# Optimization experiments

Measured on AMD Instinct MI355X. Metric: run time of the kernel, lower is better.

The kernel has to match this reference:

```python
import jax, jax.numpy as jnp
import numpy as np

V, D, B, S, T, MAXLEN = 32000, 256, 4, 512, 256, 512


def _gru(x, Wih, Whh, bih, bhh):
    """torch-style GRU over x:[B,L,Din] -> [B,L,D]. Weight rows ordered [r,z,n]."""
    Dh = Whh.shape[1]
    xW = x @ Wih.T + bih  # [B,L,3D] precompute input projections

    def step(h, xw):
        hW = h @ Whh.T + bhh
        xr, xz, xn = jnp.split(xw, 3, axis=-1)
        hr, hz, hn = jnp.split(hW, 3, axis=-1)
        r = jax.nn.sigmoid(xr + hr)
        z = jax.nn.sigmoid(xz + hz)
        n = jnp.tanh(xn + r * hn)
        h = (1.0 - z) * n + z * h
        return h, h

    h0 = jnp.zeros((x.shape[0], Dh), x.dtype)
    _, ys = jax.lax.scan(step, h0, jnp.swapaxes(xW, 0, 1))
    return jnp.swapaxes(ys, 0, 1)


def setup_inputs() -> dict:
    key = jax.random.key(0)
    ks = jax.random.split(key, 24)

    def n(k, shape, scale=0.02):
        return (jax.random.normal(k, shape, jnp.float32) * scale).astype(jnp.float32)

    inp = {
        "src": jax.random.randint(ks[0], (B, S), 0, V),
        "tgt": jax.random.randint(ks[1], (B, T), 0, V),
        "emb": n(ks[2], (V, D)),
        "pos": n(ks[3], (MAXLEN, D)),
        # encoder forward direction
        "ef_wih": n(ks[4], (3 * D, D)), "ef_whh": n(ks[5], (3 * D, D)),
        "ef_bih": n(ks[6], (3 * D,)), "ef_bhh": n(ks[7], (3 * D,)),
        # encoder backward direction
        "eb_wih": n(ks[8], (3 * D, D)), "eb_whh": n(ks[9], (3 * D, D)),
        "eb_bih": n(ks[10], (3 * D,)), "eb_bhh": n(ks[11], (3 * D,)),
        # decoder
        "d_wih": n(ks[12], (3 * D, D)), "d_whh": n(ks[13], (3 * D, D)),
        "d_bih": n(ks[14], (3 * D,)), "d_bhh": n(ks[15], (3 * D,)),
        "Wq": n(ks[16], (D, D)),
        "Wk": n(ks[17], (D, 2 * D)),
        "Wgen": n(ks[18], (V, 3 * D)), "bgen": n(ks[19], (V,)),
        "Wgate": n(ks[20], (1, 3 * D)), "bgate": n(ks[21], (1,)),
    }
    return inp


def reference(src, tgt, emb, pos,
              ef_wih, ef_whh, ef_bih, ef_bhh,
              eb_wih, eb_whh, eb_bih, eb_bhh,
              d_wih, d_whh, d_bih, d_bhh,
              Wq, Wk, Wgen, bgen, Wgate, bgate):
    b, s = src.shape
    t = tgt.shape[1]
    d = emb.shape[1]
    v = emb.shape[0]

    src_emb = emb[src] + pos[:s][None]          # [B,S,D]
    enc_f = _gru(src_emb, ef_wih, ef_whh, ef_bih, ef_bhh)
    enc_b = _gru(src_emb[:, ::-1], eb_wih, eb_whh, eb_bih, eb_bhh)[:, ::-1]
    enc_out = jnp.concatenate([enc_f, enc_b], axis=-1)  # [B,S,2D]

    tgt_emb = emb[tgt] + pos[:t][None]
    dec_out = _gru(tgt_emb, d_wih, d_whh, d_bih, d_bhh)  # [B,T,D]

    Q = dec_out @ Wq.T                           # [B,T,D]
    K = enc_out @ Wk.T                           # [B,S,D]
    scores = jnp.einsum('btd,bsd->bts', Q, K) / jnp.sqrt(jnp.asarray(d, jnp.float32))
    pos_probs = jax.nn.softmax(scores, axis=-1)  # [B,T,S]

    # copy distribution: scatter attention mass into vocab buckets (== one_hot bmm)
    P_copy = jnp.zeros((b, t, v), pos_probs.dtype).at[
        jnp.arange(b)[:, None, None],
        jnp.arange(t)[None, :, None],
        src[:, None, :],
    ].add(pos_probs)

    ctx_f = jnp.einsum('bts,bsd->btd', pos_probs, enc_f)
    ctx_b = jnp.einsum('bts,bsd->btd', pos_probs, enc_b)
    combined = jnp.concatenate([dec_out, ctx_f, ctx_b], axis=-1)  # [B,T,3D]

    P_gen = jax.nn.softmax(combined @ Wgen.T + bgen, axis=-1)     # [B,T,V]
    gate = jax.nn.sigmoid(combined @ Wgate.T + bgate)             # [B,T,1]
    return gate * P_gen + (1.0 - gate) * P_copy
```

## Files before the change

### kernel.cpp

```cpp
#include <hip/hip_runtime.h>
#include <hip/hip_bf16.h>
#include <math.h>

#define VV   32000
#define DIM  256
#define BB   4
#define SS   512
#define TT   256
#define D2   512
#define D3   768

typedef __attribute__((ext_vector_type(8))) short s16x8;
typedef __attribute__((ext_vector_type(4))) float f32x4;

__device__ __forceinline__ float rcp_(float x) { return __builtin_amdgcn_rcpf(x); }
__device__ __forceinline__ float sigmoidf_(float x) { return rcp_(1.0f + __expf(-x)); }
__device__ __forceinline__ float tanhf_(float x) {
    float t = __expf(-2.0f * x);
    return (1.0f - t) * rcp_(1.0f + t);
}
__device__ __forceinline__ short f2bf(float f) {
    unsigned u = __float_as_uint(f);
    u += 0x7FFFu + ((u >> 16) & 1u);
    return (short)(u >> 16);
}

#define BAR_LGKM() asm volatile("s_waitcnt lgkmcnt(0)\n\ts_barrier" ::: "memory")

__global__ __launch_bounds__(256) void k_embed(const int* __restrict__ src,
                                               const int* __restrict__ tgt,
                                               const float* __restrict__ emb,
                                               const float* __restrict__ pos,
                                               float* __restrict__ src_emb,
                                               float* __restrict__ tgt_emb) {
    int i = blockIdx.x * 256 + threadIdx.x;
    const int nS = BB * SS * DIM;
    if (i < nS) {
        int d = i & (DIM - 1);
        int s = (i >> 8) & (SS - 1);
        int b = i >> 17;
        src_emb[i] = emb[(size_t)src[b * SS + s] * DIM + d] + pos[s * DIM + d];
    } else {
        int j = i - nS;
        int d = j & (DIM - 1);
        int t = (j >> 8) & (TT - 1);
        int b = j >> 16;
        tgt_emb[j] = emb[(size_t)tgt[b * TT + t] * DIM + d] + pos[t * DIM + d];
    }
}

struct GDesc {
    const float* A; int lda;
    const float* Bt; int ldb;
    const float* bias;
    float* C; int ldc;
    int M, N;
};

#define BMM 128
#define BNN 128
#define BKK 8

__global__ __launch_bounds__(256) void k_gemmb(GDesc d0, GDesc d1, GDesc d2) {
    GDesc d = (blockIdx.z == 0) ? d0 : ((blockIdx.z == 1) ? d1 : d2);
    int brow = blockIdx.y * BMM, bcol = blockIdx.x * BNN;
    if (brow >= d.M || bcol >= d.N) return;

    __shared__ float As[BKK][BMM + 4];
    __shared__ float Bs[BKK][BNN + 4];
    const int K = d.lda;
    int tid = threadIdx.x;
    int tx = tid & 15, ty = tid >> 4;
    float acc[8][8];
#pragma unroll
    for (int i = 0; i < 8; i++)
#pragma unroll
        for (int j = 0; j < 8; j++) acc[i][j] = 0.0f;

    int lr = tid >> 1;
    int lk = (tid & 1) * 4;
    for (int k0 = 0; k0 < K; k0 += BKK) {
        float4 a4 = *(const float4*)&d.A[(size_t)(brow + lr) * d.lda + k0 + lk];
        float4 b4 = *(const float4*)&d.Bt[(size_t)(bcol + lr) * d.ldb + k0 + lk];
        As[lk + 0][lr] = a4.x; As[lk + 1][lr] = a4.y; As[lk + 2][lr] = a4.z; As[lk + 3][lr] = a4.w;
        Bs[lk + 0][lr] = b4.x; Bs[lk + 1][lr] = b4.y; Bs[lk + 2][lr] = b4.z; Bs[lk + 3][lr] = b4.w;
        __syncthreads();
#pragma unroll
        for (int kk = 0; kk < BKK; kk++) {
            float4 a0 = *(const float4*)&As[kk][ty * 8];
            float4 a1 = *(const float4*)&As[kk][ty * 8 + 4];
            float4 b0 = *(const float4*)&Bs[kk][tx * 8];
            float4 b1 = *(const float4*)&Bs[kk][tx * 8 + 4];
            float av[8] = {a0.x, a0.y, a0.z, a0.w, a1.x, a1.y, a1.z, a1.w};
            float bv[8] = {b0.x, b0.y, b0.z, b0.w, b1.x, b1.y, b1.z, b1.w};
#pragma unroll
            for (int i = 0; i < 8; i++)
#pragma unroll
                for (int j = 0; j < 8; j++) acc[i][j] += av[i] * bv[j];
        }
        __syncthreads();
    }

    float bv0[8];
#pragma unroll
    for (int j = 0; j < 8; j++) bv0[j] = d.bias ? d.bias[bcol + tx * 8 + j] : 0.0f;

#pragma unroll
    for (int i = 0; i < 8; i++) {
        size_t row = brow + ty * 8 + i;
        float4 c0 = make_float4(acc[i][0] + bv0[0], acc[i][1] + bv0[1],
                                acc[i][2] + bv0[2], acc[i][3] + bv0[3]);
        float4 c1 = make_float4(acc[i][4] + bv0[4], acc[i][5] + bv0[5],
                                acc[i][6] + bv0[6], acc[i][7] + bv0[7]);
        *(float4*)&d.C[row * d.ldc + bcol + tx * 8] = c0;
        *(float4*)&d.C[row * d.ldc + bcol + tx * 8 + 4] = c1;
    }
}

#define HSTRIDE 576
#define HBUF    (4 * HSTRIDE)

__global__ __launch_bounds__(512, 2) void k_gru(const float* __restrict__ ef_x,
                                                const float* __restrict__ eb_x,
                                                const float* __restrict__ d_x,
                                                const float* __restrict__ ef_whh, const float* __restrict__ ef_bhh,
                                                const float* __restrict__ eb_whh, const float* __restrict__ eb_bhh,
                                                const float* __restrict__ d_whh, const float* __restrict__ d_bhh,
                                                float* __restrict__ enc_out,
                                                float* __restrict__ dec_out) {
    __shared__ __align__(16) char hb[2 * HBUF];

    int tid = threadIdx.x;
    int dir = blockIdx.x;
    const float *xw, *Whh, *bhh;
    int L;
    if (dir == 0)      { xw = ef_x; Whh = ef_whh; bhh = ef_bhh; L = SS; }
    else if (dir == 1) { xw = eb_x; Whh = eb_whh; bhh = eb_bhh; L = SS; }
    else               { xw = d_x;  Whh = d_whh;  bhh = d_bhh;  L = TT; }

    const int wv = tid >> 6;
    const int lane = tid & 63;
    const int jj = lane & 15;
    const int hi = lane >> 4;
    const int b = hi;

    if (tid < 288) {
        f32x4 z = {0.f, 0.f, 0.f, 0.f};
        *(f32x4*)(hb + tid * 16) = z;
    }

    s16x8 wf[3][2][8];
#pragma unroll
    for (int g = 0; g < 3; ++g)
#pragma unroll
        for (int t = 0; t < 2; ++t) {
            const int nrow = g * 256 + wv * 32 + t * 16 + jj;
            const float* wp = Whh + (size_t)nrow * 256 + hi * 8;
#pragma unroll
            for (int sk = 0; sk < 8; ++sk) {
                float4 w0 = *(const float4*)(wp + sk * 32);
                float4 w1 = *(const float4*)(wp + sk * 32 + 4);
                s16x8 v;
                v[0] = f2bf(w0.x); v[1] = f2bf(w0.y); v[2] = f2bf(w0.z); v[3] = f2bf(w0.w);
                v[4] = f2bf(w1.x); v[5] = f2bf(w1.y); v[6] = f2bf(w1.z); v[7] = f2bf(w1.w);
                wf[g][t][sk] = v;
            }
        }

    const int j0 = wv * 32 + jj, j1 = j0 + 16;
    const float br0 = bhh[j0], bz0 = bhh[256 + j0], bn0 = bhh[512 + j0];
    const float br1 = bhh[j1], bz1 = bhh[256 + j1], bn1 = bhh[512 + j1];

    const int arow = jj >> 2;
    const int abase = arow * HSTRIDE + hi * 16;
    const int wo0 = b * HSTRIDE + 2 * j0;
    const int wo1 = b * HSTRIDE + 2 * j1;

    const int s0 = (dir == 1) ? (L - 1) : 0;
    const int sst = (dir == 1) ? -1 : 1;
    const float* xq = xw + ((size_t)b * L + s0) * D3 + j0;
    float* op;
    int ostride;
    if (dir == 2) { op = dec_out + ((size_t)b * TT + s0) * DIM + j0; ostride = sst * DIM; }
    else          { op = enc_out + ((size_t)b * SS + s0) * D2 + (dir == 1 ? DIM : 0) + j0; ostride = sst * D2; }
    const int xstride = sst * D3;

    float c0 = xq[0], c1 = xq[256], c2 = xq[512], c3 = xq[16], c4 = xq[272], c5 = xq[528];

    float h0 = 0.f, h1 = 0.f;
    int cur = 0;
    __syncthreads();

    for (int st = 0; st < L; ++st) {
        xq += xstride;
        float n0 = xq[0], n1 = xq[256], n2 = xq[512], n3 = xq[16], n4 = xq[272], n5 = xq[528];

        const char* hcur = hb + cur * HBUF;
        f32x4 a00 = {0.f, 0.f, 0.f, 0.f}, a01 = a00, a10 = a00, a11 = a00, a20 = a00, a21 = a00;
#pragma unroll
        for (int sk = 0; sk < 8; ++sk) {
            s16x8 af = *(const s16x8*)(hcur + abase + 64 * sk);
            a00 = __builtin_amdgcn_mfma_f32_16x16x32_bf16(af, wf[0][0][sk], a00, 0, 0, 0);
            a01 = __builtin_amdgcn_mfma_f32_16x16x32_bf16(af, wf[0][1][sk], a01, 0, 0, 0);
            a10 = __builtin_amdgcn_mfma_f32_16x16x32_bf16(af, wf[1][0][sk], a10, 0, 0, 0);
            a11 = __builtin_amdgcn_mfma_f32_16x16x32_bf16(af, wf[1][1][sk], a11, 0, 0, 0);
            a20 = __builtin_amdgcn_mfma_f32_16x16x32_bf16(af, wf[2][0][sk], a20, 0, 0, 0);
            a21 = __builtin_amdgcn_mfma_f32_16x16x32_bf16(af, wf[2][1][sk], a21, 0, 0, 0);
        }

        float r0 = sigmoidf_(c0 + a00[0] + br0);
        float z0 = sigmoidf_(c1 + a10[0] + bz0);
        float nn0 = tanhf_(c2 + r0 * (a20[0] + bn0));
        h0 = (1.f - z0) * nn0 + z0 * h0;
        float r1 = sigmoidf_(c3 + a01[0] + br1);
        float z1 = sigmoidf_(c4 + a11[0] + bz1);
        float nn1 = tanhf_(c5 + r1 * (a21[0] + bn1));
        h1 = (1.f - z1) * nn1 + z1 * h1;

        char* hnxt = hb + (cur ^ 1) * HBUF;
        *(short*)(hnxt + wo0) = f2bf(h0);
        *(short*)(hnxt + wo1) = f2bf(h1);
        op[0] = h0;
        op[16] = h1;
        BAR_LGKM();

        cur ^= 1;
        c0 = n0; c1 = n1; c2 = n2; c3 = n3; c4 = n4; c5 = n5;
        op += ostride;
    }
}

__global__ __launch_bounds__(512) void k_attn(const float* __restrict__ Qb,
                                              const float* __restrict__ Kb,
                                              const float* __restrict__ enc_out,
                                              const float* __restrict__ dec_out,
                                              const float* __restrict__ Wgate,
                                              const float* __restrict__ bgate,
                                              float* __restrict__ probs,
                                              short* __restrict__ cmb,
                                              float* __restrict__ gate) {
    __shared__ float q[DIM];
    __shared__ float sc[SS];
    __shared__ float red[512];
    __shared__ float par[2][2][DIM];
    int row = blockIdx.x;
    int b = row >> 8;
    int tid = threadIdx.x;

    if (tid < DIM) q[tid] = Qb[(size_t)row * DIM + tid];
    __syncthreads();

    const float scale = 0.0625f;
    {
        const float* kr = Kb + ((size_t)b * SS + tid) * DIM;
        float acc = 0.0f;
        for (int k = 0; k < DIM; k += 4) {
            float4 k4 = *(const float4*)&kr[k];
            acc += k4.x * q[k] + k4.y * q[k + 1] + k4.z * q[k + 2] + k4.w * q[k + 3];
        }
        sc[tid] = acc * scale;
    }
    __syncthreads();

    red[tid] = sc[tid];
    __syncthreads();
    for (int o = 256; o > 0; o >>= 1) {
        if (tid < o) red[tid] = fmaxf(red[tid], red[tid + o]);
        __syncthreads();
    }
    float m = red[0];
    __syncthreads();

    float e0 = __expf(sc[tid] - m);
    sc[tid] = e0;
    red[tid] = e0;
    __syncthreads();
    for (int o = 256; o > 0; o >>= 1) {
        if (tid < o) red[tid] += red[tid + o];
        __syncthreads();
    }
    float inv = rcp_(red[0]);
    __syncthreads();

    sc[tid] *= inv;
    probs[(size_t)row * SS + tid] = sc[tid];
    __syncthreads();

    {
        int d = tid & 255, sh = tid >> 8;
        float accf = 0.0f, accb = 0.0f;
        const float* ep = enc_out + ((size_t)b * SS + sh * 256) * D2 + d;
        const float* pp = &sc[sh * 256];
        for (int s = 0; s < 256; s++) {
            float p = pp[s];
            accf += p * ep[(size_t)s * D2];
            accb += p * ep[(size_t)s * D2 + DIM];
        }
        par[sh][0][d] = accf;
        par[sh][1][d] = accb;
    }
    __syncthreads();

    if (tid < DIM) {
        float af = par[0][0][tid] + par[1][0][tid];
        float ab = par[0][1][tid] + par[1][1][tid];
        float dv = dec_out[(size_t)row * DIM + tid];
        cmb[(size_t)row * D3 + tid] = f2bf(dv);
        cmb[(size_t)row * D3 + DIM + tid] = f2bf(af);
        cmb[(size_t)row * D3 + 2 * DIM + tid] = f2bf(ab);
        red[tid] = dv * Wgate[tid] + af * Wgate[DIM + tid] + ab * Wgate[2 * DIM + tid];
    }
    __syncthreads();
    for (int o = 128; o > 0; o >>= 1) {
        if (tid < o) red[tid] += red[tid + o];
        __syncthreads();
    }
    if (tid == 0) gate[row] = sigmoidf_(red[0] + bgate[0]);
}

__global__ __launch_bounds__(512) void k_gen(const short* __restrict__ A,
                                             const float* __restrict__ Bw,
                                             const float* __restrict__ bias,
                                             float* __restrict__ C,
                                             float* __restrict__ rowsum) {
    __shared__ __align__(16) short As[256 * 32];
    __shared__ __align__(16) short Bs[128 * 32];
    int tid = threadIdx.x;
    int lane = tid & 63, wv = tid >> 6;
    int wm = wv >> 1, wn = wv & 1;
    int brow = blockIdx.y * 256, bcol = blockIdx.x * 128;
    f32x4 acc[4][4];
#pragma unroll
    for (int i = 0; i < 4; i++)
#pragma unroll
        for (int j = 0; j < 4; j++) acc[i][j] = (f32x4){0.f, 0.f, 0.f, 0.f};

    const int ca0 = tid, ca1 = tid + 512, cb = tid;
    const int ll = lane & 15, lh = lane >> 4;

    for (int k0 = 0; k0 < D3; k0 += 32) {
        s16x8 va0 = *(const s16x8*)&A[(size_t)(brow + (ca0 >> 2)) * D3 + k0 + (ca0 & 3) * 8];
        s16x8 va1 = *(const s16x8*)&A[(size_t)(brow + (ca1 >> 2)) * D3 + k0 + (ca1 & 3) * 8];
        const float* bp = &Bw[(size_t)(bcol + (cb >> 2)) * D3 + k0 + (cb & 3) * 8];
        float4 b0 = *(const float4*)bp;
        float4 b1 = *(const float4*)(bp + 4);
        s16x8 vb;
        vb[0] = f2bf(b0.x); vb[1] = f2bf(b0.y); vb[2] = f2bf(b0.z); vb[3] = f2bf(b0.w);
        vb[4] = f2bf(b1.x); vb[5] = f2bf(b1.y); vb[6] = f2bf(b1.z); vb[7] = f2bf(b1.w);

        __syncthreads();
        *(s16x8*)&As[ca0 * 8] = va0;
        *(s16x8*)&As[ca1 * 8] = va1;
        *(s16x8*)&Bs[cb * 8] = vb;
        __syncthreads();

        s16x8 af[4], bf[4];
#pragma unroll
        for (int mt = 0; mt < 4; ++mt)
            af[mt] = *(const s16x8*)&As[(wm * 64 + mt * 16 + ll) * 32 + lh * 8];
#pragma unroll
        for (int nt = 0; nt < 4; ++nt)
            bf[nt] = *(const s16x8*)&Bs[(wn * 64 + nt * 16 + ll) * 32 + lh * 8];
#pragma unroll
        for (int mt = 0; mt < 4; ++mt)
#pragma unroll
            for (int nt = 0; nt < 4; ++nt)
                acc[mt][nt] = __builtin_amdgcn_mfma_f32_16x16x32_bf16(af[mt], bf[nt], acc[mt][nt], 0, 0, 0);
    }

#pragma unroll
    for (int nt = 0; nt < 4; ++nt) {
        float bv = bias[bcol + wn * 64 + nt * 16 + ll];
#pragma unroll
        for (int mt = 0; mt < 4; ++mt)
#pragma unroll
            for (int q = 0; q < 4; ++q) acc[mt][nt][q] += bv;
    }

#pragma unroll
    for (int mt = 0; mt < 4; ++mt) {
        int row = brow + wm * 64 + mt * 16 + lh * 4;
#pragma unroll
        for (int nt = 0; nt < 4; ++nt) {
            int col = bcol + wn * 64 + nt * 16 + ll;
#pragma unroll
            for (int q = 0; q < 4; ++q)
                C[(size_t)(row + q) * VV + col] = acc[mt][nt][q];
        }
    }

#pragma unroll
    for (int mt = 0; mt < 4; ++mt) {
#pragma unroll
        for (int q = 0; q < 4; ++q) {
            float se = __expf(acc[mt][0][q]) + __expf(acc[mt][1][q]) +
                       __expf(acc[mt][2][q]) + __expf(acc[mt][3][q]);
#pragma unroll
            for (int off = 1; off < 16; off <<= 1)
                se += __shfl_xor(se, off);
            if (ll == 0) {
                int row = brow + wm * 64 + mt * 16 + lh * 4 + q;
                atomicAdd(&rowsum[row], se);
            }
        }
    }
}

__global__ __launch_bounds__(256) void k_finsc(const int* __restrict__ src,
                                               const float* __restrict__ probs,
                                               const float* __restrict__ gate,
                                               const float* __restrict__ rowsum,
                                               float* __restrict__ out) {
    int row = blockIdx.x;
    int b = row >> 8;
    int tid = threadIdx.x;
    float g = gate[row];
    float inv = g / rowsum[row];
    float* op = out + (size_t)row * VV;

    for (int i = tid; i < VV / 4; i += 256) {
        float4 l = *(const float4*)&op[i * 4];
        l.x = __expf(l.x) * inv;
        l.y = __expf(l.y) * inv;
        l.z = __expf(l.z) * inv;
        l.w = __expf(l.w) * inv;
        *(float4*)&op[i * 4] = l;
    }
    __syncthreads();

    float og = 1.0f - g;
#pragma unroll
    for (int h = 0; h < 2; ++h) {
        int s = tid + h * 256;
        float val = og * probs[(size_t)row * SS + s];
        atomicAdd(&op[src[b * SS + s]], val);
    }
}

extern "C" void kernel_launch(void* const* d_in, const int* in_sizes, int n_in,
                              void* d_out, int out_size, void* d_ws, size_t ws_size,
                              hipStream_t stream) {
    const int*   src    = (const int*)d_in[0];
    const int*   tgt    = (const int*)d_in[1];
    const float* emb    = (const float*)d_in[2];
    const float* pos    = (const float*)d_in[3];
    const float* ef_wih = (const float*)d_in[4];
    const float* ef_whh = (const float*)d_in[5];
    const float* ef_bih = (const float*)d_in[6];
    const float* ef_bhh = (const float*)d_in[7];
    const float* eb_wih = (const float*)d_in[8];
    const float* eb_whh = (const float*)d_in[9];
    const float* eb_bih = (const float*)d_in[10];
    const float* eb_bhh = (const float*)d_in[11];
    const float* d_wih  = (const float*)d_in[12];
    const float* d_whh  = (const float*)d_in[13];
    const float* d_bih  = (const float*)d_in[14];
    const float* d_bhh  = (const float*)d_in[15];
    const float* Wq     = (const float*)d_in[16];
    const float* Wk     = (const float*)d_in[17];
    const float* Wgen   = (const float*)d_in[18];
    const float* bgen   = (const float*)d_in[19];
    const float* Wgate  = (const float*)d_in[20];
    const float* bgate  = (const float*)d_in[21];
    float* out = (float*)d_out;
    float* ws  = (float*)d_ws;

    float* src_emb  = ws;
    float* tgt_emb  = src_emb + (size_t)BB * SS * DIM;
    float* ef_x     = tgt_emb + (size_t)BB * TT * DIM;
    float* eb_x     = ef_x + (size_t)BB * SS * D3;
    float* d_x      = eb_x + (size_t)BB * SS * D3;
    float* enc_out  = d_x + (size_t)BB * TT * D3;
    float* dec_out  = enc_out + (size_t)BB * SS * D2;
    float* Qb       = dec_out + (size_t)BB * TT * DIM;
    float* Kb       = Qb + (size_t)BB * TT * DIM;
    float* probs    = Kb + (size_t)BB * SS * DIM;
    short* cmb_bf   = (short*)(probs + (size_t)BB * TT * SS);
    float* gate     = (float*)(cmb_bf + (size_t)BB * TT * D3);
    float* rowsum   = gate + 1024;

    hipMemsetAsync(rowsum, 0, 1024 * sizeof(float), stream);

    k_embed<<<(BB * SS * DIM + BB * TT * DIM) / 256, 256, 0, stream>>>(
        src, tgt, emb, pos, src_emb, tgt_emb);

    {
        GDesc e0 = {src_emb, DIM, ef_wih, DIM, ef_bih, ef_x, D3, BB * SS, D3};
        GDesc e1 = {src_emb, DIM, eb_wih, DIM, eb_bih, eb_x, D3, BB * SS, D3};
        GDesc e2 = {tgt_emb, DIM, d_wih, DIM, d_bih, d_x, D3, BB * TT, D3};
        k_gemmb<<<dim3(D3 / BNN, BB * SS / BMM, 3), 256, 0, stream>>>(e0, e1, e2);
    }

    k_gru<<<3, 512, 0, stream>>>(ef_x, eb_x, d_x, ef_whh, ef_bhh, eb_whh, eb_bhh,
                                 d_whh, d_bhh, enc_out, dec_out);

    {
        GDesc q0 = {dec_out, DIM, Wq, DIM, nullptr, Qb, DIM, BB * TT, DIM};
        GDesc q1 = {enc_out, D2, Wk, D2, nullptr, Kb, DIM, BB * SS, DIM};
        k_gemmb<<<dim3(DIM / BNN, BB * SS / BMM, 2), 256, 0, stream>>>(q0, q1, q1);
    }

    k_attn<<<BB * TT, 512, 0, stream>>>(Qb, Kb, enc_out, dec_out, Wgate, bgate,
                                        probs, cmb_bf, gate);

    k_gen<<<dim3(VV / 128, (BB * TT) / 256), 512, 0, stream>>>(cmb_bf, Wgen, bgen, out, rowsum);

    k_finsc<<<BB * TT, 256, 0, stream>>>(src, probs, gate, rowsum, out);
}
```

Measured before the change: 1.161 ms.

## Use bf16 MFMA for input projections and pre-convert Wgen to bf16

Replaces the fp32 SIMT GEMM for the three GRU input projections with a bf16 MFMA kernel that converts operands while staging them into shared memory. It also adds a kernel that converts Wgen to bf16 once per call into workspace, so the vocab-generation GEMM loads half as many bytes per weight tile and skips in-loop conversion. The bf16 path runs only when the workspace is large enough, and it costs an extra pass over Wgen plus lower precision in the projections.

```diff
diff --git a/kernel.cpp b/kernel.cpp
--- a/kernel.cpp
+++ b/kernel.cpp
@@ -49,6 +49,18 @@
     }
 }
 
+__global__ __launch_bounds__(256) void k_cvt(const float* __restrict__ in,
+                                             short* __restrict__ outp, int n8) {
+    int i = blockIdx.x * 256 + threadIdx.x;
+    if (i >= n8) return;
+    const float4* p = (const float4*)(in + (size_t)i * 8);
+    float4 a = p[0], b = p[1];
+    s16x8 v;
+    v[0] = f2bf(a.x); v[1] = f2bf(a.y); v[2] = f2bf(a.z); v[3] = f2bf(a.w);
+    v[4] = f2bf(b.x); v[5] = f2bf(b.y); v[6] = f2bf(b.z); v[7] = f2bf(b.w);
+    *(s16x8*)(outp + (size_t)i * 8) = v;
+}
+
 struct GDesc {
     const float* A; int lda;
     const float* Bt; int ldb;
@@ -114,6 +126,87 @@
                                 acc[i][6] + bv0[6], acc[i][7] + bv0[7]);
         *(float4*)&d.C[row * d.ldc + bcol + tx * 8] = c0;
         *(float4*)&d.C[row * d.ldc + bcol + tx * 8 + 4] = c1;
+    }
+}
+
+struct PDesc {
+    const float* A;
+    const float* Bt;
+    const float* bias;
+    float* C;
+    int M;
+};
+
+__global__ __launch_bounds__(512) void k_proj(PDesc p0, PDesc p1, PDesc p2) {
+    PDesc p = (blockIdx.z == 0) ? p0 : ((blockIdx.z == 1) ? p1 : p2);
+    int brow = blockIdx.y * 256;
+    if (brow >= p.M) return;
+    int bcol = blockIdx.x * 128;
+
+    __shared__ __align__(16) short As[256 * 32];
+    __shared__ __align__(16) short Bs[128 * 32];
+    int tid = threadIdx.x;
+    int lane = tid & 63, wv = tid >> 6;
+    int wm = wv >> 1, wn = wv & 1;
+    const int ll = lane & 15, lh = lane >> 4;
+
+    f32x4 acc[4][4];
+#pragma unroll
+    for (int i = 0; i < 4; i++)
+#pragma unroll
+        for (int j = 0; j < 4; j++) acc[i][j] = (f32x4){0.f, 0.f, 0.f, 0.f};
+
+    const int ar = tid >> 1, ak = (tid & 1) * 16;
+    const int br = tid >> 2, bk = (tid & 3) * 8;
+
+    for (int k0 = 0; k0 < DIM; k0 += 32) {
+        const float* ap = &p.A[(size_t)(brow + ar) * DIM + k0 + ak];
+        float4 a0 = *(const float4*)ap;
+        float4 a1 = *(const float4*)(ap + 4);
+        float4 a2 = *(const float4*)(ap + 8);
+        float4 a3 = *(const float4*)(ap + 12);
+        const float* bp = &p.Bt[(size_t)(bcol + br) * DIM + k0 + bk];
+        float4 b0 = *(const float4*)bp;
+        float4 b1 = *(const float4*)(bp + 4);
+        s16x8 va0, va1, vb;
+        va0[0] = f2bf(a0.x); va0[1] = f2bf(a0.y); va0[2] = f2bf(a0.z); va0[3] = f2bf(a0.w);
+        va0[4] = f2bf(a1.x); va0[5] = f2bf(a1.y); va0[6] = f2bf(a1.z); va0[7] = f2bf(a1.w);
+        va1[0] = f2bf(a2.x); va1[1] = f2bf(a2.y); va1[2] = f2bf(a2.z); va1[3] = f2bf(a2.w);
+        va1[4] = f2bf(a3.x); va1[5] = f2bf(a3.y); va1[6] = f2bf(a3.z); va1[7] = f2bf(a3.w);
+        vb[0] = f2bf(b0.x); vb[1] = f2bf(b0.y); vb[2] = f2bf(b0.z); vb[3] = f2bf(b0.w);
+        vb[4] = f2bf(b1.x); vb[5] = f2bf(b1.y); vb[6] = f2bf(b1.z); vb[7] = f2bf(b1.w);
+
+        __syncthreads();
+        *(s16x8*)&As[ar * 32 + ak] = va0;
+        *(s16x8*)&As[ar * 32 + ak + 8] = va1;
+        *(s16x8*)&Bs[br * 32 + bk] = vb;
+        __syncthreads();
+
+        s16x8 af[4], bf[4];
+#pragma unroll
+        for (int mt = 0; mt < 4; ++mt)
+            af[mt] = *(const s16x8*)&As[(wm * 64 + mt * 16 + ll) * 32 + lh * 8];
+#pragma unroll
+        for (int nt = 0; nt < 4; ++nt)
+            bf[nt] = *(const s16x8*)&Bs[(wn * 64 + nt * 16 + ll) * 32 + lh * 8];
+#pragma unroll
+        for (int mt = 0; mt < 4; ++mt)
+#pragma unroll
+            for (int nt = 0; nt < 4; ++nt)
+                acc[mt][nt] = __builtin_amdgcn_mfma_f32_16x16x32_bf16(af[mt], bf[nt], acc[mt][nt], 0, 0, 0);
+    }
+
+#pragma unroll
+    for (int mt = 0; mt < 4; ++mt) {
+        int row = brow + wm * 64 + mt * 16 + lh * 4;
+#pragma unroll
+        for (int nt = 0; nt < 4; ++nt) {
+            int col = bcol + wn * 64 + nt * 16 + ll;
+            float bv = p.bias[col];
+#pragma unroll
+            for (int q = 0; q < 4; ++q)
+                p.C[(size_t)(row + q) * D3 + col] = acc[mt][nt][q] + bv;
+        }
     }
 }
 
@@ -316,6 +409,89 @@
         __syncthreads();
     }
     if (tid == 0) gate[row] = sigmoidf_(red[0] + bgate[0]);
+}
+
+__global__ __launch_bounds__(512) void k_gen_bf(const short* __restrict__ A,
+                                                const short* __restrict__ Bbf,
+                                                const float* __restrict__ bias,
+                                                float* __restrict__ C,
+                                                float* __restrict__ rowsum) {
+    __shared__ __align__(16) short As[256 * 32];
+    __shared__ __align__(16) short Bs[128 * 32];
+    int tid = threadIdx.x;
+    int lane = tid & 63, wv = tid >> 6;
+    int wm = wv >> 1, wn = wv & 1;
+    int brow = blockIdx.y * 256, bcol = blockIdx.x * 128;
+    f32x4 acc[4][4];
+#pragma unroll
+    for (int i = 0; i < 4; i++)
+#pragma unroll
+        for (int j = 0; j < 4; j++) acc[i][j] = (f32x4){0.f, 0.f, 0.f, 0.f};
+
+    const int ca0 = tid, ca1 = tid + 512, cb = tid;
+    const int ll = lane & 15, lh = lane >> 4;
+
+    for (int k0 = 0; k0 < D3; k0 += 32) {
+        s16x8 va0 = *(const s16x8*)&A[(size_t)(brow + (ca0 >> 2)) * D3 + k0 + (ca0 & 3) * 8];
+        s16x8 va1 = *(const s16x8*)&A[(size_t)(brow + (ca1 >> 2)) * D3 + k0 + (ca1 & 3) * 8];
+        s16x8 vb  = *(const s16x8*)&Bbf[(size_t)(bcol + (cb >> 2)) * D3 + k0 + (cb & 3) * 8];
+
+        __syncthreads();
+        *(s16x8*)&As[ca0 * 8] = va0;
+        *(s16x8*)&As[ca1 * 8] = va1;
+        *(s16x8*)&Bs[cb * 8] = vb;
+        __syncthreads();
+
+        s16x8 af[4], bf[4];
+#pragma unroll
+        for (int mt = 0; mt < 4; ++mt)
+            af[mt] = *(const s16x8*)&As[(wm * 64 + mt * 16 + ll) * 32 + lh * 8];
+#pragma unroll
+        for (int nt = 0; nt < 4; ++nt)
+            bf[nt] = *(const s16x8*)&Bs[(wn * 64 + nt * 16 + ll) * 32 + lh * 8];
+#pragma unroll
+        for (int mt = 0; mt < 4; ++mt)
+#pragma unroll
+            for (int nt = 0; nt < 4; ++nt)
+                acc[mt][nt] = __builtin_amdgcn_mfma_f32_16x16x32_bf16(af[mt], bf[nt], acc[mt][nt], 0, 0, 0);
+    }
+
+#pragma unroll
+    for (int nt = 0; nt < 4; ++nt) {
+        float bv = bias[bcol + wn * 64 + nt * 16 + ll];
+#pragma unroll
+        for (int mt = 0; mt < 4; ++mt)
+#pragma unroll
+            for (int q = 0; q < 4; ++q) acc[mt][nt][q] += bv;
+    }
+
+#pragma unroll
+    for (int mt = 0; mt < 4; ++mt) {
+        int row = brow + wm * 64 + mt * 16 + lh * 4;
+#pragma unroll
+        for (int nt = 0; nt < 4; ++nt) {
+            int col = bcol + wn * 64 + nt * 16 + ll;
+#pragma unroll
+            for (int q = 0; q < 4; ++q)
+                C[(size_t)(row + q) * VV + col] = acc[mt][nt][q];
+        }
+    }
+
+#pragma unroll
+    for (int mt = 0; mt < 4; ++mt) {
+#pragma unroll
+        for (int q = 0; q < 4; ++q) {
+            float se = __expf(acc[mt][0][q]) + __expf(acc[mt][1][q]) +
+                       __expf(acc[mt][2][q]) + __expf(acc[mt][3][q]);
+#pragma unroll
+            for (int off = 1; off < 16; off <<= 1)
+                se += __shfl_xor(se, off);
+            if (ll == 0) {
+                int row = brow + wm * 64 + mt * 16 + lh * 4 + q;
+                atomicAdd(&rowsum[row], se);
+            }
+        }
+    }
 }
 
 __global__ __launch_bounds__(512) void k_gen(const short* __restrict__ A,
@@ -478,17 +654,22 @@
     short* cmb_bf   = (short*)(probs + (size_t)BB * TT * SS);
     float* gate     = (float*)(cmb_bf + (size_t)BB * TT * D3);
     float* rowsum   = gate + 1024;
+    short* wgen_bf  = (short*)(rowsum + 1024);
+    const bool use_bf = ws_size >= (size_t)((char*)(wgen_bf + (size_t)VV * D3) - (char*)d_ws);
 
     hipMemsetAsync(rowsum, 0, 1024 * sizeof(float), stream);
 
     k_embed<<<(BB * SS * DIM + BB * TT * DIM) / 256, 256, 0, stream>>>(
         src, tgt, emb, pos, src_emb, tgt_emb);
 
+    if (use_bf)
+        k_cvt<<<(VV * D3 / 8 + 255) / 256, 256, 0, stream>>>(Wgen, wgen_bf, VV * D3 / 8);
+
     {
-        GDesc e0 = {src_emb, DIM, ef_wih, DIM, ef_bih, ef_x, D3, BB * SS, D3};
-        GDesc e1 = {src_emb, DIM, eb_wih, DIM, eb_bih, eb_x, D3, BB * SS, D3};
-        GDesc e2 = {tgt_emb, DIM, d_wih, DIM, d_bih, d_x, D3, BB * TT, D3};
-        k_gemmb<<<dim3(D3 / BNN, BB * SS / BMM, 3), 256, 0, stream>>>(e0, e1, e2);
+        PDesc e0 = {src_emb, ef_wih, ef_bih, ef_x, BB * SS};
+        PDesc e1 = {src_emb, eb_wih, eb_bih, eb_x, BB * SS};
+        PDesc e2 = {tgt_emb, d_wih, d_bih, d_x, BB * TT};
+        k_proj<<<dim3(D3 / 128, BB * SS / 256, 3), 512, 0, stream>>>(e0, e1, e2);
     }
 
     k_gru<<<3, 512, 0, stream>>>(ef_x, eb_x, d_x, ef_whh, ef_bhh, eb_whh, eb_bhh,
@@ -503,7 +684,10 @@
     k_attn<<<BB * TT, 512, 0, stream>>>(Qb, Kb, enc_out, dec_out, Wgate, bgate,
                                         probs, cmb_bf, gate);
 
-    k_gen<<<dim3(VV / 128, (BB * TT) / 256), 512, 0, stream>>>(cmb_bf, Wgen, bgen, out, rowsum);
+    if (use_bf)
+        k_gen_bf<<<dim3(VV / 128, (BB * TT) / 256), 512, 0, stream>>>(cmb_bf, wgen_bf, bgen, out, rowsum);
+    else
+        k_gen<<<dim3(VV / 128, (BB * TT) / 256), 512, 0, stream>>>(cmb_bf, Wgen, bgen, out, rowsum);
 
     k_finsc<<<BB * TT, 256, 0, stream>>>(src, probs, gate, rowsum, out);
 }
```

After: 1.142 ms. About the same (-1.6%).
